# Performance work log

Measured on AMD Instinct MI355X. Metric: run time of the kernel, lower is better.

## Reference

```python
import jax, jax.numpy as jnp
import numpy as np

NEG_SLOPE = 0.2


def gat_layer(h, src, dst, W, al, ar, b, num_nodes):
    # h: [N, Din], W: [Din, H*F], al/ar: [H, F], b: [H*F]
    H, F = al.shape
    feat = (h @ W).reshape(-1, H, F)                      # [N, H, F]
    el = jnp.sum(feat * al[None], axis=-1)                # [N, H]
    er = jnp.sum(feat * ar[None], axis=-1)                # [N, H]
    e = el[src] + er[dst]                                 # [E, H]
    e = jnp.where(e > 0, e, NEG_SLOPE * e)                # leaky_relu(0.2)
    # edge softmax over incoming edges of each dst node (per head)
    m = jax.ops.segment_max(e, dst, num_segments=num_nodes)   # [N, H]
    m = jnp.where(jnp.isfinite(m), m, 0.0)
    a = jnp.exp(e - m[dst])                               # [E, H]
    s = jax.ops.segment_sum(a, dst, num_segments=num_nodes)   # [N, H]
    alpha = a / jnp.maximum(s[dst], 1e-9)                 # [E, H]
    msg = feat[src] * alpha[:, :, None]                   # [E, H, F]
    out = jax.ops.segment_sum(msg, dst, num_segments=num_nodes)  # [N, H, F]
    out = out + b.reshape(H, F)[None]
    return out.reshape(-1, H * F)                         # view(-1, H*F)


def setup_inputs() -> dict:
    key = jax.random.key(0)
    ks = jax.random.split(key, 16)
    N, E, Din, Hh, F = 50000, 800000, 256, 4, 64
    s = 0.05
    return {
        "h": jax.random.normal(ks[0], (N, Din), jnp.float32),
        "src": jax.random.randint(ks[1], (E,), 0, N),
        "dst": jax.random.randint(ks[2], (E,), 0, N),
        "dst_node_ids": jax.random.randint(ks[3], (1024,), 0, N),
        "W0": jax.random.normal(ks[4], (Din, Hh * F), jnp.float32) * s,
        "al0": jax.random.normal(ks[5], (Hh, F), jnp.float32) * s,
        "ar0": jax.random.normal(ks[6], (Hh, F), jnp.float32) * s,
        "b0": jnp.zeros((Hh * F,), jnp.float32),
        "W1": jax.random.normal(ks[7], (Hh * F, Hh * F), jnp.float32) * s,
        "al1": jax.random.normal(ks[8], (Hh, F), jnp.float32) * s,
        "ar1": jax.random.normal(ks[9], (Hh, F), jnp.float32) * s,
        "b1": jnp.zeros((Hh * F,), jnp.float32),
        "W2": jax.random.normal(ks[10], (Hh * F, F), jnp.float32) * s,
        "al2": jax.random.normal(ks[11], (1, F), jnp.float32) * s,
        "ar2": jax.random.normal(ks[12], (1, F), jnp.float32) * s,
        "b2": jnp.zeros((F,), jnp.float32),
    }


def reference(h, src, dst, dst_node_ids,
              W0, al0, ar0, b0, W1, al1, ar1, b1, W2, al2, ar2, b2):
    N = h.shape[0]
    h = h.astype(jnp.float32)
    h = gat_layer(h, src, dst, W0, al0, ar0, b0, N)
    h = gat_layer(h, src, dst, W1, al1, ar1, b1, N)
    h = gat_layer(h, src, dst, W2, al2, ar2, b2, N)
    return h, dst_node_ids
```

## Files before the change

### kernel.cpp

```cpp
#include <hip/hip_runtime.h>
#include <hip/hip_bf16.h>

#define NEG_SLOPE 0.2f

typedef __attribute__((ext_vector_type(8))) short bf16x8;
typedef __attribute__((ext_vector_type(4))) float f32x4;

static inline int cdiv(int a, int b) { return (a + b - 1) / b; }

__device__ inline unsigned short f2bf(float x) {
  __hip_bfloat16 b = __float2bfloat16(x);
  return *reinterpret_cast<unsigned short*>(&b);
}
__device__ inline float bf2f(unsigned short u) {
  unsigned int v = (unsigned int)u << 16;
  return *reinterpret_cast<float*>(&v);
}

__global__ void splitT_all(const float* __restrict__ W0, unsigned short* __restrict__ W0hi,
                           const float* __restrict__ W1, unsigned short* __restrict__ W1hi,
                           const float* __restrict__ W2, unsigned short* __restrict__ W2hi) {
  const int S0 = 256 * 256, S1 = 256 * 256, S2 = 256 * 64;
  int i = blockIdx.x * blockDim.x + threadIdx.x;
  const float* W; unsigned short* hi; int K, Mo, perm;
  if (i < S0) { W = W0; hi = W0hi; K = 256; Mo = 256; perm = 0; }
  else if (i < S0 + S1) { i -= S0; W = W1; hi = W1hi; K = 256; Mo = 256; perm = 1; }
  else if (i < S0 + S1 + S2) { i -= S0 + S1; W = W2; hi = W2hi; K = 256; Mo = 64; perm = 1; }
  else return;
  int k = i / Mo, m = i - k * Mo;
  int kk = perm ? ((k & 63) * 4 + (k >> 6)) : k;
  hi[(size_t)m * K + kk] = f2bf(W[i]);
}

template <int NF, bool CVT>
__global__ __launch_bounds__(256) void gemm_split(
    const unsigned short* __restrict__ Ahi, const float* __restrict__ Af32,
    const unsigned short* __restrict__ BThi,
    unsigned short* __restrict__ Chi, signed char* __restrict__ Cq,
    const float* __restrict__ alv, const float* __restrict__ arv,
    float* __restrict__ elsc, float* __restrict__ er4,
    float* __restrict__ el1, float* __restrict__ er1,
    int M, int K, int Ncols) {
  constexpr int BN = NF * 32;
  __shared__ unsigned short As[128][40];
  __shared__ unsigned short Bs[BN][40];
  const int tid = threadIdx.x;
  const int row0 = blockIdx.x * 128;
  const int col0 = blockIdx.y * BN;
  const int wid = tid >> 6, lane = tid & 63;
  const int wm = wid >> 1, wn = wid & 1;
  const int l15 = lane & 15, lg = lane >> 4;
  f32x4 acc[4][NF];
#pragma unroll
  for (int m = 0; m < 4; ++m)
#pragma unroll
    for (int n = 0; n < NF; ++n) acc[m][n] = (f32x4){0.f, 0.f, 0.f, 0.f};

  const uint4 zero4 = {0u, 0u, 0u, 0u};
  for (int k0 = 0; k0 < K; k0 += 32) {
    {
      int r = tid >> 2;
      const int kg = tid & 3;
#pragma unroll
      for (int it = 0; it < 2; ++it, r += 64) {
        const int grow = row0 + r;
        if constexpr (CVT) {
          float4 f0 = make_float4(0.f, 0.f, 0.f, 0.f), f1 = f0;
          if (grow < M) {
            f0 = *reinterpret_cast<const float4*>(&Af32[(size_t)grow * K + k0 + kg * 8]);
            f1 = *reinterpret_cast<const float4*>(&Af32[(size_t)grow * K + k0 + kg * 8 + 4]);
          }
          unsigned short t[8];
          t[0] = f2bf(f0.x); t[1] = f2bf(f0.y); t[2] = f2bf(f0.z); t[3] = f2bf(f0.w);
          t[4] = f2bf(f1.x); t[5] = f2bf(f1.y); t[6] = f2bf(f1.z); t[7] = f2bf(f1.w);
          *reinterpret_cast<uint4*>(&As[r][kg * 8]) = *reinterpret_cast<const uint4*>(t);
        } else {
          uint4 vh = zero4;
          if (grow < M) vh = *reinterpret_cast<const uint4*>(&Ahi[(size_t)grow * K + k0 + kg * 8]);
          *reinterpret_cast<uint4*>(&As[r][kg * 8]) = vh;
        }
      }
    }
    {
      int r = tid >> 2;
      const int kg = tid & 3;
#pragma unroll
      for (int it = 0; it < BN / 64; ++it, r += 64) {
        const int gcol = col0 + r;
        uint4 vh = *reinterpret_cast<const uint4*>(&BThi[(size_t)gcol * K + k0 + kg * 8]);
        *reinterpret_cast<uint4*>(&Bs[r][kg * 8]) = vh;
      }
    }
    __syncthreads();
    bf16x8 ah[4];
#pragma unroll
    for (int m = 0; m < 4; ++m) {
      const int row = wm * 64 + m * 16 + l15;
      ah[m] = *reinterpret_cast<const bf16x8*>(&As[row][lg * 8]);
    }
#pragma unroll
    for (int n = 0; n < NF; ++n) {
      const int col = wn * (NF * 16) + n * 16 + l15;
      bf16x8 bh = *reinterpret_cast<const bf16x8*>(&Bs[col][lg * 8]);
#pragma unroll
      for (int m = 0; m < 4; ++m)
        acc[m][n] = __builtin_amdgcn_mfma_f32_16x16x32_bf16(ah[m], bh, acc[m][n], 0, 0, 0);
    }
    __syncthreads();
  }
  const int hw = (col0 + wn * (NF * 16)) >> 6;
  float alw[NF], arw[NF];
#pragma unroll
  for (int n = 0; n < NF; ++n) {
    const int colg = col0 + wn * (NF * 16) + n * 16 + l15;
    alw[n] = alv[colg];
    arw[n] = arv[colg];
  }

  if constexpr (NF == 4) {
#pragma unroll
    for (int m = 0; m < 4; ++m) {
#pragma unroll
      for (int j = 0; j < 4; ++j) {
        float mx = 0.f, vl = 0.f, vr = 0.f;
#pragma unroll
        for (int n = 0; n < 4; ++n) {
          const float v = acc[m][n][j];
          mx = fmaxf(mx, fabsf(v));
          vl = fmaf(v, alw[n], vl);
          vr = fmaf(v, arw[n], vr);
        }
#pragma unroll
        for (int off = 1; off < 16; off <<= 1) {
          mx = fmaxf(mx, __shfl_xor(mx, off));
          vl += __shfl_xor(vl, off);
          vr += __shfl_xor(vr, off);
        }
        const int row = row0 + wm * 64 + m * 16 + lg * 4 + j;
        if (row < M) {
          const float rinv = mx > 0.f ? 127.f / mx : 0.f;
#pragma unroll
          for (int n = 0; n < 4; ++n) {
            const int f = n * 16 + l15;
            const int q = __float2int_rn(acc[m][n][j] * rinv);
            Cq[(size_t)row * 256 + (f << 2) + hw] = (signed char)q;
          }
          if (l15 == 0) {
            elsc[(size_t)row * 8 + hw] = vl;
            elsc[(size_t)row * 8 + 4 + hw] = mx * (1.f / 127.f);
            er4[(size_t)row * 4 + hw] = vr;
          }
        }
      }
    }
  } else {
    float pel[4][4] = {{0.f}}, per_[4][4] = {{0.f}};
#pragma unroll
    for (int m = 0; m < 4; ++m) {
#pragma unroll
      for (int n = 0; n < NF; ++n) {
        const int col = col0 + wn * (NF * 16) + n * 16 + l15;
#pragma unroll
        for (int j = 0; j < 4; ++j) {
          const int row = row0 + wm * 64 + m * 16 + lg * 4 + j;
          const float v = acc[m][n][j];
          if (row < M) Chi[(size_t)row * Ncols + col] = f2bf(v);
          pel[m][j] = fmaf(v, alw[n], pel[m][j]);
          per_[m][j] = fmaf(v, arw[n], per_[m][j]);
        }
      }
    }
    float rl[4][4], rr[4][4];
#pragma unroll
    for (int m = 0; m < 4; ++m) {
#pragma unroll
      for (int j = 0; j < 4; ++j) {
        float vl = pel[m][j], vr = per_[m][j];
#pragma unroll
        for (int off = 1; off < 16; off <<= 1) {
          vl += __shfl_xor(vl, off);
          vr += __shfl_xor(vr, off);
        }
        rl[m][j] = vl; rr[m][j] = vr;
      }
    }
    __shared__ float sl[128], sr[128];
    if (wn == 1 && l15 == 0) {
#pragma unroll
      for (int m = 0; m < 4; ++m)
#pragma unroll
        for (int j = 0; j < 4; ++j) {
          const int lr = wm * 64 + m * 16 + lg * 4 + j;
          sl[lr] = rl[m][j]; sr[lr] = rr[m][j];
        }
    }
    __syncthreads();
    if (wn == 0 && l15 == 0) {
#pragma unroll
      for (int m = 0; m < 4; ++m)
#pragma unroll
        for (int j = 0; j < 4; ++j) {
          const int lr = wm * 64 + m * 16 + lg * 4 + j;
          const int row = row0 + lr;
          if (row < M) {
            el1[row] = rl[m][j] + sl[lr];
            er1[row] = rr[m][j] + sr[lr];
          }
        }
    }
  }
}

__global__ void hist_kernel(const int* __restrict__ dst, int* __restrict__ deg, int E) {
  int i = blockIdx.x * blockDim.x + threadIdx.x;
  if (i < E) atomicAdd(&deg[dst[i]], 1);
}

__global__ void scan1(const int* __restrict__ deg, int* __restrict__ offs,
                      int* __restrict__ bsums, int N) {
  __shared__ int tmp[256];
  const int tid = threadIdx.x;
  const int i = blockIdx.x * 256 + tid;
  int v = (i < N) ? deg[i] : 0;
  tmp[tid] = v;
  __syncthreads();
  for (int d = 1; d < 256; d <<= 1) {
    int t = (tid >= d) ? tmp[tid - d] : 0;
    __syncthreads();
    tmp[tid] += t;
    __syncthreads();
  }
  if (i < N) offs[i] = tmp[tid] - v;
  if (tid == 255) bsums[blockIdx.x] = tmp[255];
}

__global__ void scan2(int* __restrict__ bsums, int nb) {
  __shared__ int tmp[256];
  const int tid = threadIdx.x;
  int v = (tid < nb) ? bsums[tid] : 0;
  tmp[tid] = v;
  __syncthreads();
  for (int d = 1; d < 256; d <<= 1) {
    int t = (tid >= d) ? tmp[tid - d] : 0;
    __syncthreads();
    tmp[tid] += t;
    __syncthreads();
  }
  if (tid < nb) bsums[tid] = tmp[tid] - v;
}

__global__ void scan3(int* __restrict__ offs, const int* __restrict__ bsums,
                      int* __restrict__ cursor, int N, int E) {
  const int i = blockIdx.x * 256 + threadIdx.x;
  if (i < N) {
    const int v = offs[i] + bsums[blockIdx.x];
    offs[i] = v;
    cursor[i] = v;
  }
  if (i == 0) offs[N] = E;
}

__global__ void scatter_kernel(const int* __restrict__ src, const int* __restrict__ dst,
                               int* __restrict__ cursor, int* __restrict__ csr_src, int E) {
  int i = blockIdx.x * blockDim.x + threadIdx.x;
  if (i >= E) return;
  int pos = atomicAdd(&cursor[dst[i]], 1);
  csr_src[pos] = src[i];
}

__global__ void alpha16_h4(const int* __restrict__ offs, const int* __restrict__ csr_src,
                           const float* __restrict__ elsc, const float* __restrict__ er4,
                           unsigned short* __restrict__ abuf, int N) {
  const int w = (int)((blockIdx.x * (size_t)blockDim.x + threadIdx.x) >> 6);
  const int lane = threadIdx.x & 63;
  const int g = lane >> 4, q = lane & 15;
  const int node = w * 4 + g;
  int beg = 0, end = 0;
  float erh[4] = {0.f, 0.f, 0.f, 0.f};
  if (node < N) {
    beg = offs[node]; end = offs[node + 1];
    float4 t = *reinterpret_cast<const float4*>(&er4[(size_t)node * 4]);
    erh[0] = t.x; erh[1] = t.y; erh[2] = t.z; erh[3] = t.w;
  }
  float m[4], s[4];
#pragma unroll
  for (int h = 0; h < 4; ++h) { m[h] = -INFINITY; s[h] = 0.f; }
  for (int i0 = beg; i0 < end; i0 += 16) {
    const int i = i0 + q;
    const bool valid = i < end;
    const int sn = valid ? csr_src[i] : 0;
    float4 v = *reinterpret_cast<const float4*>(&elsc[(size_t)sn * 8]);
    float e[4] = {v.x + erh[0], v.y + erh[1], v.z + erh[2], v.w + erh[3]};
#pragma unroll
    for (int h = 0; h < 4; ++h) {
      e[h] = e[h] > 0.f ? e[h] : NEG_SLOPE * e[h];
      if (!valid) e[h] = -INFINITY;
      float cm = e[h];
#pragma unroll
      for (int off = 1; off < 16; off <<= 1) cm = fmaxf(cm, __shfl_xor(cm, off));
      const float nm = fmaxf(m[h], cm);
      float cs = __expf(e[h] - nm);
#pragma unroll
      for (int off = 1; off < 16; off <<= 1) cs += __shfl_xor(cs, off);
      s[h] = s[h] * __expf(m[h] - nm) + cs;
      m[h] = nm;
    }
  }
  float inv[4];
#pragma unroll
  for (int h = 0; h < 4; ++h) inv[h] = 1.f / fmaxf(s[h], 1e-9f);
  for (int i0 = beg; i0 < end; i0 += 16) {
    const int i = i0 + q;
    if (i < end) {
      const int sn = csr_src[i];
      float4 v = *reinterpret_cast<const float4*>(&elsc[(size_t)sn * 8]);
      float4 sc = *reinterpret_cast<const float4*>(&elsc[(size_t)sn * 8 + 4]);
      float e[4] = {v.x + erh[0], v.y + erh[1], v.z + erh[2], v.w + erh[3]};
      const float scv[4] = {sc.x, sc.y, sc.z, sc.w};
#pragma unroll
      for (int h = 0; h < 4; ++h) {
        e[h] = e[h] > 0.f ? e[h] : NEG_SLOPE * e[h];
        e[h] = __expf(e[h] - m[h]) * inv[h] * scv[h];
      }
      ushort4 o;
      o.x = f2bf(e[0]); o.y = f2bf(e[1]); o.z = f2bf(e[2]); o.w = f2bf(e[3]);
      *reinterpret_cast<ushort4*>(&abuf[(size_t)i * 4]) = o;
    }
  }
}

__global__ void alpha16_h1(const int* __restrict__ offs, const int* __restrict__ csr_src,
                           const float* __restrict__ el, const float* __restrict__ er,
                           unsigned short* __restrict__ abuf, int N) {
  const int w = (int)((blockIdx.x * (size_t)blockDim.x + threadIdx.x) >> 6);
  const int lane = threadIdx.x & 63;
  const int g = lane >> 4, q = lane & 15;
  const int node = w * 4 + g;
  int beg = 0, end = 0;
  float erh = 0.f;
  if (node < N) { beg = offs[node]; end = offs[node + 1]; erh = er[node]; }
  float m = -INFINITY, s = 0.f;
  for (int i0 = beg; i0 < end; i0 += 16) {
    const int i = i0 + q;
    const bool valid = i < end;
    const int sn = valid ? csr_src[i] : 0;
    float e = el[sn] + erh;
    e = e > 0.f ? e : NEG_SLOPE * e;
    if (!valid) e = -INFINITY;
    float cm = e;
#pragma unroll
    for (int off = 1; off < 16; off <<= 1) cm = fmaxf(cm, __shfl_xor(cm, off));
    const float nm = fmaxf(m, cm);
    float cs = __expf(e - nm);
#pragma unroll
    for (int off = 1; off < 16; off <<= 1) cs += __shfl_xor(cs, off);
    s = s * __expf(m - nm) + cs;
    m = nm;
  }
  const float inv = 1.f / fmaxf(s, 1e-9f);
  for (int i0 = beg; i0 < end; i0 += 16) {
    const int i = i0 + q;
    if (i < end) {
      const int sn = csr_src[i];
      float e = el[sn] + erh;
      e = e > 0.f ? e : NEG_SLOPE * e;
      abuf[i] = f2bf(__expf(e - m) * inv);
    }
  }
}

__global__ void aggregate_h4(const int* __restrict__ offs, const int* __restrict__ csr_src,
                             const unsigned* __restrict__ qtab, const ushort4* __restrict__ abuf4,
                             const float* __restrict__ bias, ushort4* __restrict__ out4, int N) {
  const int node = (int)((blockIdx.x * (size_t)blockDim.x + threadIdx.x) >> 6);
  const int lane = threadIdx.x & 63;
  if (node >= N) return;
  const int beg = offs[node], end = offs[node + 1];
  float a0 = 0.f, a1 = 0.f, a2 = 0.f, a3 = 0.f;
  int i = beg;
  for (; i + 7 < end; i += 8) {
    int sn[8]; ushort4 w[8]; unsigned qw[8];
#pragma unroll
    for (int u = 0; u < 8; ++u) sn[u] = csr_src[i + u];
#pragma unroll
    for (int u = 0; u < 8; ++u) w[u] = abuf4[i + u];
#pragma unroll
    for (int u = 0; u < 8; ++u) qw[u] = qtab[(size_t)sn[u] * 64 + lane];
#pragma unroll
    for (int u = 0; u < 8; ++u) {
      a0 = fmaf(bf2f(w[u].x), (float)(int)(signed char)(qw[u] & 0xff), a0);
      a1 = fmaf(bf2f(w[u].y), (float)(int)(signed char)((qw[u] >> 8) & 0xff), a1);
      a2 = fmaf(bf2f(w[u].z), (float)(int)(signed char)((qw[u] >> 16) & 0xff), a2);
      a3 = fmaf(bf2f(w[u].w), (float)(int)(signed char)(qw[u] >> 24), a3);
    }
  }
  for (; i < end; ++i) {
    const int sn = csr_src[i];
    const ushort4 w = abuf4[i];
    const unsigned qw = qtab[(size_t)sn * 64 + lane];
    a0 = fmaf(bf2f(w.x), (float)(int)(signed char)(qw & 0xff), a0);
    a1 = fmaf(bf2f(w.y), (float)(int)(signed char)((qw >> 8) & 0xff), a1);
    a2 = fmaf(bf2f(w.z), (float)(int)(signed char)((qw >> 16) & 0xff), a2);
    a3 = fmaf(bf2f(w.w), (float)(int)(signed char)(qw >> 24), a3);
  }
  const float o0 = a0 + bias[lane];
  const float o1 = a1 + bias[64 + lane];
  const float o2 = a2 + bias[128 + lane];
  const float o3 = a3 + bias[192 + lane];
  ushort4 ov;
  ov.x = f2bf(o0); ov.y = f2bf(o1); ov.z = f2bf(o2); ov.w = f2bf(o3);
  out4[(size_t)node * 64 + lane] = ov;
}

__global__ void aggregate1(const int* __restrict__ offs, const int* __restrict__ csr_src,
                           const unsigned short* __restrict__ featH, const unsigned short* __restrict__ abuf,
                           const float* __restrict__ bias, float* __restrict__ outf, int N) {
  const int wid = (int)((blockIdx.x * (size_t)blockDim.x + threadIdx.x) >> 6);
  const int lane = threadIdx.x & 63;
  if (wid >= N) return;
  const int beg = offs[wid], end = offs[wid + 1];
  const int g = lane >> 4, q = lane & 15;
  float4 acc = make_float4(0.f, 0.f, 0.f, 0.f);
  for (int i0 = beg; i0 < end; i0 += 4) {
    const int e = i0 + g;
    if (e < end) {
      const int sn = csr_src[e];
      const float a = bf2f(abuf[e]);
      const ushort4 u = *reinterpret_cast<const ushort4*>(&featH[(size_t)sn * 64 + q * 4]);
      acc.x = fmaf(a, bf2f(u.x), acc.x);
      acc.y = fmaf(a, bf2f(u.y), acc.y);
      acc.z = fmaf(a, bf2f(u.z), acc.z);
      acc.w = fmaf(a, bf2f(u.w), acc.w);
    }
  }
#pragma unroll
  for (int off = 16; off <= 32; off <<= 1) {
    acc.x += __shfl_xor(acc.x, off);
    acc.y += __shfl_xor(acc.y, off);
    acc.z += __shfl_xor(acc.z, off);
    acc.w += __shfl_xor(acc.w, off);
  }
  if (lane < 16) {
    const float4 b4 = *reinterpret_cast<const float4*>(&bias[q * 4]);
    float4 o = make_float4(acc.x + b4.x, acc.y + b4.y, acc.z + b4.z, acc.w + b4.w);
    *reinterpret_cast<float4*>(&outf[(size_t)wid * 64 + q * 4]) = o;
  }
}

__global__ void copy_ids(const int* __restrict__ ids, float* __restrict__ out, int n) {
  int i = blockIdx.x * blockDim.x + threadIdx.x;
  if (i < n) out[i] = (float)ids[i];
}

extern "C" void kernel_launch(void* const* d_in, const int* in_sizes, int n_in,
                              void* d_out, int out_size, void* d_ws, size_t ws_size,
                              hipStream_t stream) {
  const float* h   = (const float*)d_in[0];
  const int* src   = (const int*)d_in[1];
  const int* dst   = (const int*)d_in[2];
  const int* ids   = (const int*)d_in[3];
  const float* W0  = (const float*)d_in[4];
  const float* al0 = (const float*)d_in[5];
  const float* ar0 = (const float*)d_in[6];
  const float* b0  = (const float*)d_in[7];
  const float* W1  = (const float*)d_in[8];
  const float* al1 = (const float*)d_in[9];
  const float* ar1 = (const float*)d_in[10];
  const float* b1  = (const float*)d_in[11];
  const float* W2  = (const float*)d_in[12];
  const float* al2 = (const float*)d_in[13];
  const float* ar2 = (const float*)d_in[14];
  const float* b2  = (const float*)d_in[15];

  const int Din = 256, HF = 256, F2 = 64;
  const int N = in_sizes[0] / Din;
  const int E = in_sizes[1];
  const int NIDS = in_sizes[3];

  char* p = (char*)d_ws;
  signed char* Cq = (signed char*)p;   p += (size_t)N * 256;
  unsigned short* Chi = (unsigned short*)p; p += (size_t)N * 64 * 2;
  unsigned short* Ahi = (unsigned short*)p; p += (size_t)N * 256 * 2;
  unsigned short* W0hi = (unsigned short*)p; p += (size_t)HF * Din * 2;
  unsigned short* W1hi = (unsigned short*)p; p += (size_t)HF * HF * 2;
  unsigned short* W2hi = (unsigned short*)p; p += (size_t)F2 * HF * 2;
  float* elsc = (float*)p;             p += (size_t)N * 8 * 4;
  float* er4  = (float*)p;             p += (size_t)N * 4 * 4;
  float* el1  = (float*)p;             p += (size_t)N * 4;
  float* er1  = (float*)p;             p += (size_t)N * 4;
  unsigned short* abuf = (unsigned short*)p; p += (size_t)E * 4 * 2;
  int* deg    = (int*)p;               p += (size_t)N * 4;
  int* offs   = (int*)p;               p += (size_t)(N + 16) * 4;
  int* bsums  = (int*)p;               p += 256 * 4;
  int* csr_src = (int*)p;              p += (size_t)E * 4;

  float* outp = (float*)d_out;
  dim3 blk(256);
  const int nb = cdiv(N, 256);
  const int nwAlpha = cdiv(cdiv(N, 4) * 64, 256);

  splitT_all<<<cdiv(256 * 256 * 2 + 256 * 64, 256), blk, 0, stream>>>(
      W0, W0hi, W1, W1hi, W2, W2hi);

  hipMemsetAsync(deg, 0, (size_t)N * 4, stream);
  hist_kernel<<<cdiv(E, 256), blk, 0, stream>>>(dst, deg, E);
  scan1<<<nb, blk, 0, stream>>>(deg, offs, bsums, N);
  scan2<<<1, blk, 0, stream>>>(bsums, nb);
  scan3<<<nb, blk, 0, stream>>>(offs, bsums, deg, N, E);
  scatter_kernel<<<cdiv(E, 256), blk, 0, stream>>>(src, dst, deg, csr_src, E);

  {
    dim3 g(cdiv(N, 128), HF / 128);
    gemm_split<4, true><<<g, blk, 0, stream>>>(nullptr, h, W0hi, nullptr, Cq, al0, ar0,
                                               elsc, er4, nullptr, nullptr, N, Din, HF);
    alpha16_h4<<<nwAlpha, blk, 0, stream>>>(offs, csr_src, elsc, er4, abuf, N);
    aggregate_h4<<<cdiv(N * 64, 256), blk, 0, stream>>>(offs, csr_src, (const unsigned*)Cq,
                                                        (const ushort4*)abuf, b0, (ushort4*)Ahi, N);
  }
  {
    dim3 g(cdiv(N, 128), HF / 128);
    gemm_split<4, false><<<g, blk, 0, stream>>>(Ahi, nullptr, W1hi, nullptr, Cq, al1, ar1,
                                                elsc, er4, nullptr, nullptr, N, HF, HF);
    alpha16_h4<<<nwAlpha, blk, 0, stream>>>(offs, csr_src, elsc, er4, abuf, N);
    aggregate_h4<<<cdiv(N * 64, 256), blk, 0, stream>>>(offs, csr_src, (const unsigned*)Cq,
                                                        (const ushort4*)abuf, b1, (ushort4*)Ahi, N);
  }
  {
    dim3 g(cdiv(N, 128), 1);
    gemm_split<2, false><<<g, blk, 0, stream>>>(Ahi, nullptr, W2hi, Chi, nullptr, al2, ar2,
                                                nullptr, nullptr, el1, er1, N, HF, F2);
    alpha16_h1<<<nwAlpha, blk, 0, stream>>>(offs, csr_src, el1, er1, abuf, N);
    aggregate1<<<cdiv(N * 64, 256), blk, 0, stream>>>(offs, csr_src, Chi, abuf, b2, outp, N);
  }
  copy_ids<<<cdiv(NIDS, 256), blk, 0, stream>>>(ids, outp + (size_t)N * F2, NIDS);
}
```

Before: 361.8 us.

## Halve GEMM row tile and partition CSR build atomics by destination range

The GEMM kernel gets a row-fragment template parameter and every layer now runs with 64-row tiles instead of 128. This doubles the block count on 50k rows to improve occupancy and wave balance, at the cost of more reloads of the weight tile. The histogram and scatter kernels are replaced by partitioned versions. Each block handles only the destinations in one of 8 interleaved node ranges, aiming to keep atomics within an L2-friendly subset, but every edge's dst is now read 8 times.

```diff
diff --git a/kernel.cpp b/kernel.cpp
--- a/kernel.cpp
+++ b/kernel.cpp
@@ -32,7 +32,7 @@
   hi[(size_t)m * K + kk] = f2bf(W[i]);
 }
 
-template <int NF, bool CVT>
+template <int MF, int NF, bool CVT>
 __global__ __launch_bounds__(256) void gemm_split(
     const unsigned short* __restrict__ Ahi, const float* __restrict__ Af32,
     const unsigned short* __restrict__ BThi,
@@ -41,18 +41,19 @@
     float* __restrict__ elsc, float* __restrict__ er4,
     float* __restrict__ el1, float* __restrict__ er1,
     int M, int K, int Ncols) {
+  constexpr int BM = MF * 32;
   constexpr int BN = NF * 32;
-  __shared__ unsigned short As[128][40];
+  __shared__ unsigned short As[BM][40];
   __shared__ unsigned short Bs[BN][40];
   const int tid = threadIdx.x;
-  const int row0 = blockIdx.x * 128;
+  const int row0 = blockIdx.x * BM;
   const int col0 = blockIdx.y * BN;
   const int wid = tid >> 6, lane = tid & 63;
   const int wm = wid >> 1, wn = wid & 1;
   const int l15 = lane & 15, lg = lane >> 4;
-  f32x4 acc[4][NF];
-#pragma unroll
-  for (int m = 0; m < 4; ++m)
+  f32x4 acc[MF][NF];
+#pragma unroll
+  for (int m = 0; m < MF; ++m)
 #pragma unroll
     for (int n = 0; n < NF; ++n) acc[m][n] = (f32x4){0.f, 0.f, 0.f, 0.f};
 
@@ -62,7 +63,7 @@
       int r = tid >> 2;
       const int kg = tid & 3;
 #pragma unroll
-      for (int it = 0; it < 2; ++it, r += 64) {
+      for (int it = 0; it < BM / 64; ++it, r += 64) {
         const int grow = row0 + r;
         if constexpr (CVT) {
           float4 f0 = make_float4(0.f, 0.f, 0.f, 0.f), f1 = f0;
@@ -92,10 +93,10 @@
       }
     }
     __syncthreads();
-    bf16x8 ah[4];
-#pragma unroll
-    for (int m = 0; m < 4; ++m) {
-      const int row = wm * 64 + m * 16 + l15;
+    bf16x8 ah[MF];
+#pragma unroll
+    for (int m = 0; m < MF; ++m) {
+      const int row = wm * (MF * 16) + m * 16 + l15;
       ah[m] = *reinterpret_cast<const bf16x8*>(&As[row][lg * 8]);
     }
 #pragma unroll
@@ -103,7 +104,7 @@
       const int col = wn * (NF * 16) + n * 16 + l15;
       bf16x8 bh = *reinterpret_cast<const bf16x8*>(&Bs[col][lg * 8]);
 #pragma unroll
-      for (int m = 0; m < 4; ++m)
+      for (int m = 0; m < MF; ++m)
         acc[m][n] = __builtin_amdgcn_mfma_f32_16x16x32_bf16(ah[m], bh, acc[m][n], 0, 0, 0);
     }
     __syncthreads();
@@ -119,7 +120,7 @@
 
   if constexpr (NF == 4) {
 #pragma unroll
-    for (int m = 0; m < 4; ++m) {
+    for (int m = 0; m < MF; ++m) {
 #pragma unroll
       for (int j = 0; j < 4; ++j) {
         float mx = 0.f, vl = 0.f, vr = 0.f;
@@ -136,7 +137,7 @@
           vl += __shfl_xor(vl, off);
           vr += __shfl_xor(vr, off);
         }
-        const int row = row0 + wm * 64 + m * 16 + lg * 4 + j;
+        const int row = row0 + wm * (MF * 16) + m * 16 + lg * 4 + j;
         if (row < M) {
           const float rinv = mx > 0.f ? 127.f / mx : 0.f;
 #pragma unroll
@@ -154,15 +155,15 @@
       }
     }
   } else {
-    float pel[4][4] = {{0.f}}, per_[4][4] = {{0.f}};
-#pragma unroll
-    for (int m = 0; m < 4; ++m) {
+    float pel[MF][4] = {{0.f}}, per_[MF][4] = {{0.f}};
+#pragma unroll
+    for (int m = 0; m < MF; ++m) {
 #pragma unroll
       for (int n = 0; n < NF; ++n) {
         const int col = col0 + wn * (NF * 16) + n * 16 + l15;
 #pragma unroll
         for (int j = 0; j < 4; ++j) {
-          const int row = row0 + wm * 64 + m * 16 + lg * 4 + j;
+          const int row = row0 + wm * (MF * 16) + m * 16 + lg * 4 + j;
           const float v = acc[m][n][j];
           if (row < M) Chi[(size_t)row * Ncols + col] = f2bf(v);
           pel[m][j] = fmaf(v, alw[n], pel[m][j]);
@@ -170,9 +171,9 @@
         }
       }
     }
-    float rl[4][4], rr[4][4];
-#pragma unroll
-    for (int m = 0; m < 4; ++m) {
+    float rl[MF][4], rr[MF][4];
+#pragma unroll
+    for (int m = 0; m < MF; ++m) {
 #pragma unroll
       for (int j = 0; j < 4; ++j) {
         float vl = pel[m][j], vr = per_[m][j];
@@ -184,23 +185,23 @@
         rl[m][j] = vl; rr[m][j] = vr;
       }
     }
-    __shared__ float sl[128], sr[128];
+    __shared__ float sl[BM], sr[BM];
     if (wn == 1 && l15 == 0) {
 #pragma unroll
-      for (int m = 0; m < 4; ++m)
+      for (int m = 0; m < MF; ++m)
 #pragma unroll
         for (int j = 0; j < 4; ++j) {
-          const int lr = wm * 64 + m * 16 + lg * 4 + j;
+          const int lr = wm * (MF * 16) + m * 16 + lg * 4 + j;
           sl[lr] = rl[m][j]; sr[lr] = rr[m][j];
         }
     }
     __syncthreads();
     if (wn == 0 && l15 == 0) {
 #pragma unroll
-      for (int m = 0; m < 4; ++m)
+      for (int m = 0; m < MF; ++m)
 #pragma unroll
         for (int j = 0; j < 4; ++j) {
-          const int lr = wm * 64 + m * 16 + lg * 4 + j;
+          const int lr = wm * (MF * 16) + m * 16 + lg * 4 + j;
           const int row = row0 + lr;
           if (row < M) {
             el1[row] = rl[m][j] + sl[lr];
@@ -211,9 +212,14 @@
   }
 }
 
-__global__ void hist_kernel(const int* __restrict__ dst, int* __restrict__ deg, int E) {
-  int i = blockIdx.x * blockDim.x + threadIdx.x;
-  if (i < E) atomicAdd(&deg[dst[i]], 1);
+__global__ void hist_part(const int* __restrict__ dst, int* __restrict__ deg, int E) {
+  const int part = blockIdx.x & 7;
+  const int chunk = blockIdx.x >> 3;
+  const int nchunk = gridDim.x >> 3;
+  for (int i = chunk * 256 + threadIdx.x; i < E; i += nchunk * 256) {
+    const int d = dst[i];
+    if (((d >> 10) & 7) == part) atomicAdd(&deg[d], 1);
+  }
 }
 
 __global__ void scan1(const int* __restrict__ deg, int* __restrict__ offs,
@@ -260,12 +266,18 @@
   if (i == 0) offs[N] = E;
 }
 
-__global__ void scatter_kernel(const int* __restrict__ src, const int* __restrict__ dst,
-                               int* __restrict__ cursor, int* __restrict__ csr_src, int E) {
-  int i = blockIdx.x * blockDim.x + threadIdx.x;
-  if (i >= E) return;
-  int pos = atomicAdd(&cursor[dst[i]], 1);
-  csr_src[pos] = src[i];
+__global__ void scatter_part(const int* __restrict__ src, const int* __restrict__ dst,
+                             int* __restrict__ cursor, int* __restrict__ csr_src, int E) {
+  const int part = blockIdx.x & 7;
+  const int chunk = blockIdx.x >> 3;
+  const int nchunk = gridDim.x >> 3;
+  for (int i = chunk * 256 + threadIdx.x; i < E; i += nchunk * 256) {
+    const int d = dst[i];
+    if (((d >> 10) & 7) == part) {
+      const int pos = atomicAdd(&cursor[d], 1);
+      csr_src[pos] = src[i];
+    }
+  }
 }
 
 __global__ void alpha16_h4(const int* __restrict__ offs, const int* __restrict__ csr_src,
@@ -498,37 +510,38 @@
   dim3 blk(256);
   const int nb = cdiv(N, 256);
   const int nwAlpha = cdiv(cdiv(N, 4) * 64, 256);
+  const int nbPart = 8 * 96;
 
   splitT_all<<<cdiv(256 * 256 * 2 + 256 * 64, 256), blk, 0, stream>>>(
       W0, W0hi, W1, W1hi, W2, W2hi);
 
   hipMemsetAsync(deg, 0, (size_t)N * 4, stream);
-  hist_kernel<<<cdiv(E, 256), blk, 0, stream>>>(dst, deg, E);
+  hist_part<<<nbPart, blk, 0, stream>>>(dst, deg, E);
   scan1<<<nb, blk, 0, stream>>>(deg, offs, bsums, N);
   scan2<<<1, blk, 0, stream>>>(bsums, nb);
   scan3<<<nb, blk, 0, stream>>>(offs, bsums, deg, N, E);
-  scatter_kernel<<<cdiv(E, 256), blk, 0, stream>>>(src, dst, deg, csr_src, E);
+  scatter_part<<<nbPart, blk, 0, stream>>>(src, dst, deg, csr_src, E);
 
   {
-    dim3 g(cdiv(N, 128), HF / 128);
-    gemm_split<4, true><<<g, blk, 0, stream>>>(nullptr, h, W0hi, nullptr, Cq, al0, ar0,
-                                               elsc, er4, nullptr, nullptr, N, Din, HF);
+    dim3 g(cdiv(N, 64), HF / 128);
+    gemm_split<2, 4, true><<<g, blk, 0, stream>>>(nullptr, h, W0hi, nullptr, Cq, al0, ar0,
+                                                  elsc, er4, nullptr, nullptr, N, Din, HF);
     alpha16_h4<<<nwAlpha, blk, 0, stream>>>(offs, csr_src, elsc, er4, abuf, N);
     aggregate_h4<<<cdiv(N * 64, 256), blk, 0, stream>>>(offs, csr_src, (const unsigned*)Cq,
                                                         (const ushort4*)abuf, b0, (ushort4*)Ahi, N);
   }
   {
-    dim3 g(cdiv(N, 128), HF / 128);
-    gemm_split<4, false><<<g, blk, 0, stream>>>(Ahi, nullptr, W1hi, nullptr, Cq, al1, ar1,
-                                                elsc, er4, nullptr, nullptr, N, HF, HF);
+    dim3 g(cdiv(N, 64), HF / 128);
+    gemm_split<2, 4, false><<<g, blk, 0, stream>>>(Ahi, nullptr, W1hi, nullptr, Cq, al1, ar1,
+                                                   elsc, er4, nullptr, nullptr, N, HF, HF);
     alpha16_h4<<<nwAlpha, blk, 0, stream>>>(offs, csr_src, elsc, er4, abuf, N);
     aggregate_h4<<<cdiv(N * 64, 256), blk, 0, stream>>>(offs, csr_src, (const unsigned*)Cq,
                                                         (const ushort4*)abuf, b1, (ushort4*)Ahi, N);
   }
   {
-    dim3 g(cdiv(N, 128), 1);
-    gemm_split<2, false><<<g, blk, 0, stream>>>(Ahi, nullptr, W2hi, Chi, nullptr, al2, ar2,
-                                                nullptr, nullptr, el1, er1, N, HF, F2);
+    dim3 g(cdiv(N, 64), 1);
+    gemm_split<2, 2, false><<<g, blk, 0, stream>>>(Ahi, nullptr, W2hi, Chi, nullptr, al2, ar2,
+                                                   nullptr, nullptr, el1, er1, N, HF, F2);
     alpha16_h1<<<nwAlpha, blk, 0, stream>>>(offs, csr_src, el1, er1, abuf, N);
     aggregate1<<<cdiv(N * 64, 256), blk, 0, stream>>>(offs, csr_src, Chi, abuf, b2, outp, N);
   }
```

New measurement: 330.6 us. -8.6%, faster.
